# Optimization experiments

Hardware: AMD Instinct MI355X
Metric: run time of the kernel (lower is better)

## Reference

```python
import jax, jax.numpy as jnp
import numpy as np

B, S, D_IN, D_OUT = 4, 2048, 4096, 4096


def setup_inputs() -> dict:
    key = jax.random.key(0)
    k1, k2, k3, k4 = jax.random.split(key, 4)
    x = jax.random.normal(k1, (B, S, D_IN), dtype=jnp.float32) * 0.02
    base = jax.random.normal(k2, (D_IN, D_OUT), dtype=jnp.float32) * 0.02
    # mask holds the sign bits of the weight delta: 1 -> +1, 0 -> -1
    mask = jax.random.randint(k3, (D_IN, D_OUT), 0, 2, dtype=jnp.int32)
    # coeff = mean(|diff|); a small positive scalar
    coeff = jnp.abs(jax.random.normal(k4, (), dtype=jnp.float32)) * 0.01
    return {"x": x, "base": base, "coeff": coeff, "mask": mask}


def reference(x, base, coeff, mask):
    # binary_bmm(x, packed_mask) == x @ sign, sign = 2*mask - 1 in {-1, +1}
    sign = (2 * mask - 1).astype(x.dtype)            # [D_IN, D_OUT]
    return x @ base + coeff * (x @ sign)             # [B, S, D_OUT]
```

## Files before the change

kernel.cpp:

```cpp
#include <hip/hip_runtime.h>
#include <hip/hip_bf16.h>
#include <stdint.h>

#define M_DIM 8192
#define K_DIM 4096
#define N_DIM 4096
#define NT (K_DIM / 64)

typedef __attribute__((ext_vector_type(8))) short short8;
typedef __attribute__((ext_vector_type(4))) float f32x4;
typedef unsigned short ushort_t;

typedef const __attribute__((address_space(1))) unsigned int as1const_u32;
typedef __attribute__((address_space(3))) unsigned int as3_u32;

__device__ __forceinline__ unsigned short f2bf(float f) {
  unsigned int u = __float_as_uint(f);
  u += 0x7FFF + ((u >> 16) & 1);
  return (unsigned short)(u >> 16);
}

__global__ void cvt_x_kernel(const float* __restrict__ x,
                             ushort_t* __restrict__ xb, long n8) {
  long i = (long)blockIdx.x * blockDim.x + threadIdx.x;
  long stride = (long)gridDim.x * blockDim.x;
  for (; i < n8; i += stride) {
    const float4* p = (const float4*)(x + i * 8);
    float4 v0 = p[0], v1 = p[1];
    short8 o;
    o[0] = (short)f2bf(v0.x); o[1] = (short)f2bf(v0.y);
    o[2] = (short)f2bf(v0.z); o[3] = (short)f2bf(v0.w);
    o[4] = (short)f2bf(v1.x); o[5] = (short)f2bf(v1.y);
    o[6] = (short)f2bf(v1.z); o[7] = (short)f2bf(v1.w);
    *(short8*)(xb + i * 8) = o;
  }
}

__global__ void make_wt_kernel(const float* __restrict__ base,
                               const int* __restrict__ mask,
                               const float* __restrict__ coeffp,
                               ushort_t* __restrict__ wt) {
  __shared__ ushort_t tile[32][33];
  const float c = *coeffp;
  const int n0 = blockIdx.x * 32, k0 = blockIdx.y * 32;
  const int tx = threadIdx.x, ty = threadIdx.y;
#pragma unroll
  for (int r = 0; r < 4; ++r) {
    int k = k0 + ty + r * 8;
    int n = n0 + tx;
    size_t idx = (size_t)k * N_DIM + n;
    float s = mask[idx] ? c : -c;
    tile[ty + r * 8][tx] = f2bf(base[idx] + s);
  }
  __syncthreads();
#pragma unroll
  for (int r = 0; r < 4; ++r) {
    int n = n0 + ty + r * 8;
    int k = k0 + tx;
    wt[(size_t)n * K_DIM + k] = tile[tx][ty + r * 8];
  }
}

#define FENCE asm volatile("" ::: "memory")
#define BAR   do { FENCE; __builtin_amdgcn_s_barrier(); FENCE; } while (0)
#define VW6   asm volatile("s_waitcnt vmcnt(6)" ::: "memory")
#define VW4   asm volatile("s_waitcnt vmcnt(4)" ::: "memory")
#define VW0   asm volatile("s_waitcnt vmcnt(0)" ::: "memory")

__global__ __launch_bounds__(512, 2) void gemm_bf16_256(
    const ushort_t* __restrict__ Xb,
    const ushort_t* __restrict__ Wt,
    float* __restrict__ out) {
  __shared__ ushort_t Al[2][256][64];
  __shared__ ushort_t Bl[2][256][64];

  const int tid = threadIdx.x;
  const int lane = tid & 63;
  const int w = tid >> 6;
  const int wm = w >> 2, wn = w & 3;
  const int lrow = lane & 15, kg = lane >> 4;

  const int bid = blockIdx.x;
  const int swz = (bid & 7) * 64 + (bid >> 3);
  const int bm = (swz >> 4) * 256;
  const int bn = (swz & 15) * 256;

  const int rh0 = w * 8 + (lane >> 3);
  const int srcslot = (lane & 7) ^ ((lane >> 3) & 7);
  const ushort_t* Ag = Xb + (size_t)(bm + rh0) * K_DIM + srcslot * 8;
  const ushort_t* Bg = Wt + (size_t)(bn + rh0) * K_DIM + srcslot * 8;
  char* AlB = (char*)&Al[0][0][0];
  char* BlB = (char*)&Bl[0][0][0];
  const int ldsw = w * 1024;

#define STAGE(Og, Lb, u, h) do {                                                   \
    const ushort_t* _s0 = (Og) + (size_t)((h) * 128) * K_DIM + (size_t)(u) * 64;   \
    __builtin_amdgcn_global_load_lds((as1const_u32*)_s0,                           \
        (as3_u32*)((Lb) + ((u) & 1) * 32768 + (h) * 16384 + ldsw), 16, 0, 0);      \
    __builtin_amdgcn_global_load_lds((as1const_u32*)(_s0 + (size_t)64 * K_DIM),    \
        (as3_u32*)((Lb) + ((u) & 1) * 32768 + (h) * 16384 + ldsw + 8192), 16, 0, 0); \
  } while (0)

  const int arow = (wm * 16 + lrow) << 7;
  const int brow = (wn * 16 + lrow) << 7;
  const int sw0 = ((0 + kg) ^ (lrow & 7)) << 4;
  const int sw1 = ((4 + kg) ^ (lrow & 7)) << 4;

#define LDA(bt, mi, kk) (*(const short8*)(AlB + (bt) * 32768 + (mi) * 4096 + arow + ((kk) ? sw1 : sw0)))
#define LDB(bt, ni, kk) (*(const short8*)(BlB + (bt) * 32768 + (ni) * 8192 + brow + ((kk) ? sw1 : sw0)))
#define MFMA(a, b, c) __builtin_amdgcn_mfma_f32_16x16x32_bf16(a, b, c, 0, 0, 0)

  short8 Ar0[4][2], Ar1[4][2];
  short8 Br0[2][2], Br1[2][2];
  f32x4 acc[8][4] = {};

#define RD_A(dst, bt, base)                                                        \
  _Pragma("unroll")                                                                \
  for (int mi = 0; mi < 4; ++mi) {                                                 \
    dst[mi][0] = LDA(bt, (base) + mi, 0); dst[mi][1] = LDA(bt, (base) + mi, 1);    \
  }
#define RD_B(dst, bt, base)                                                        \
  _Pragma("unroll")                                                                \
  for (int ni = 0; ni < 2; ++ni) {                                                 \
    dst[ni][0] = LDB(bt, (base) + ni, 0); dst[ni][1] = LDB(bt, (base) + ni, 1);    \
  }
#define MMQ(mb, nb, Aset, Bset)                                                    \
  _Pragma("unroll")                                                                \
  for (int mi = 0; mi < 4; ++mi)                                                   \
    _Pragma("unroll")                                                              \
    for (int ni = 0; ni < 2; ++ni) {                                               \
      acc[(mb) + mi][(nb) + ni] = MFMA(Aset[mi][0], Bset[ni][0], acc[(mb) + mi][(nb) + ni]); \
      acc[(mb) + mi][(nb) + ni] = MFMA(Aset[mi][1], Bset[ni][1], acc[(mb) + mi][(nb) + ni]); \
    }

  STAGE(Ag, AlB, 0, 0); STAGE(Bg, BlB, 0, 0);
  STAGE(Bg, BlB, 0, 1); STAGE(Ag, AlB, 0, 1);
  STAGE(Ag, AlB, 1, 0); STAGE(Bg, BlB, 1, 0);
  VW4; BAR;
  RD_A(Ar0, 0, 0);
  RD_B(Br0, 0, 0);

  for (int t = 0; t < NT - 2; ++t) {
    const int bt = t & 1, bo = bt ^ 1;

    RD_B(Br1, bt, 2);
    STAGE(Bg, BlB, t + 1, 1);
    BAR;
    __builtin_amdgcn_s_setprio(1);
    MMQ(0, 0, Ar0, Br0);
    __builtin_amdgcn_s_setprio(0);
    VW6; BAR;

    RD_A(Ar1, bt, 4);
    STAGE(Ag, AlB, t + 1, 1);
    BAR;
    __builtin_amdgcn_s_setprio(1);
    MMQ(0, 2, Ar0, Br1);
    __builtin_amdgcn_s_setprio(0);
    VW6; BAR;

    STAGE(Ag, AlB, t + 2, 0);
    BAR;
    __builtin_amdgcn_s_setprio(1);
    MMQ(4, 0, Ar1, Br0);
    __builtin_amdgcn_s_setprio(0);
    RD_A(Ar0, bo, 0);
    BAR;

    STAGE(Bg, BlB, t + 2, 0);
    BAR;
    __builtin_amdgcn_s_setprio(1);
    MMQ(4, 2, Ar1, Br1);
    __builtin_amdgcn_s_setprio(0);
    VW6;
    RD_B(Br0, bo, 0);
    BAR;
  }

  STAGE(Bg, BlB, NT - 1, 1);
  STAGE(Ag, AlB, NT - 1, 1);
  VW0; BAR;
  {
    const int bt = (NT - 2) & 1, bl = (NT - 1) & 1;
    RD_B(Br1, bt, 2);
    RD_A(Ar1, bt, 4);
    MMQ(0, 0, Ar0, Br0);
    MMQ(0, 2, Ar0, Br1);
    MMQ(4, 0, Ar1, Br0);
    MMQ(4, 2, Ar1, Br1);
    RD_A(Ar0, bl, 0);
    RD_B(Br0, bl, 0);
    RD_B(Br1, bl, 2);
    RD_A(Ar1, bl, 4);
    MMQ(0, 0, Ar0, Br0);
    MMQ(0, 2, Ar0, Br1);
    MMQ(4, 0, Ar1, Br0);
    MMQ(4, 2, Ar1, Br1);
  }

#pragma unroll
  for (int mi = 0; mi < 8; ++mi)
#pragma unroll
    for (int ni = 0; ni < 4; ++ni) {
      const int gr = bm + mi * 32 + wm * 16 + kg * 4;
      const int gc = bn + ni * 64 + wn * 16 + lrow;
      float* o = out + (size_t)gr * N_DIM + gc;
#pragma unroll
      for (int r = 0; r < 4; ++r) o[(size_t)r * N_DIM] = acc[mi][ni][r];
    }
}

__global__ void gemm_f32_fallback(const float* __restrict__ x,
                                  const float* __restrict__ base,
                                  const float* __restrict__ coeffp,
                                  const int* __restrict__ mask,
                                  float* __restrict__ out) {
  __shared__ float As[32][33];
  __shared__ float Bs[32][33];
  const float c = *coeffp;
  const int tx = threadIdx.x, ty = threadIdx.y;
  const int row = blockIdx.y * 32 + ty, col = blockIdx.x * 32 + tx;
  float acc = 0.f;
  for (int kt = 0; kt < K_DIM; kt += 32) {
    As[ty][tx] = x[(size_t)row * K_DIM + kt + tx];
    size_t bidx = (size_t)(kt + ty) * N_DIM + col;
    Bs[ty][tx] = base[bidx] + (mask[bidx] ? c : -c);
    __syncthreads();
#pragma unroll
    for (int k = 0; k < 32; ++k) acc += As[ty][k] * Bs[k][tx];
    __syncthreads();
  }
  out[(size_t)row * N_DIM + col] = acc;
}

extern "C" void kernel_launch(void* const* d_in, const int* in_sizes, int n_in,
                              void* d_out, int out_size, void* d_ws, size_t ws_size,
                              hipStream_t stream) {
  const float* x     = (const float*)d_in[0];
  const float* base  = (const float*)d_in[1];
  const float* coeff = (const float*)d_in[2];
  const int*   mask  = (const int*)d_in[3];
  float* out = (float*)d_out;

  const size_t xb_bytes = (size_t)M_DIM * K_DIM * sizeof(ushort_t);
  const size_t wt_bytes = (size_t)K_DIM * N_DIM * sizeof(ushort_t);

  if (ws_size >= xb_bytes + wt_bytes) {
    ushort_t* xb = (ushort_t*)d_ws;
    ushort_t* wt = (ushort_t*)((char*)d_ws + xb_bytes);
    long n8 = (long)M_DIM * K_DIM / 8;
    cvt_x_kernel<<<4096, 256, 0, stream>>>(x, xb, n8);
    make_wt_kernel<<<dim3(N_DIM / 32, K_DIM / 32), dim3(32, 8), 0, stream>>>(base, mask, coeff, wt);
    gemm_bf16_256<<<512, 512, 0, stream>>>(xb, wt, out);
  } else {
    gemm_f32_fallback<<<dim3(N_DIM / 32, M_DIM / 32), dim3(32, 32), 0, stream>>>(x, base, coeff, mask, out);
  }
}
```

Baseline: 341.4 us.

## Restructure GEMM main loop to a simpler double-buffered schedule with fewer barriers

Replaces the four-phase interleaved schedule, where each quarter of the MFMA work sat between its own stage and barrier, with a per-iteration schedule. Each iteration reads all A/B fragments for the current buffer, runs half of the MFMAs, waits on lgkmcnt and one barrier, issues all global-to-LDS loads for tile t+2, then runs the remaining MFMAs. The prologue preloads two full tiles and the epilogue is split around a vmcnt(0) wait. This cuts the barriers per iteration from eight to two and reduces fine-grained waits. In exchange, LDS reads and global loads overlap with MFMA work at coarser granularity, which may expose more LDS latency.

```diff
diff --git a/kernel.cpp b/kernel.cpp
--- a/kernel.cpp
+++ b/kernel.cpp
@@ -63,9 +63,9 @@
 
 #define FENCE asm volatile("" ::: "memory")
 #define BAR   do { FENCE; __builtin_amdgcn_s_barrier(); FENCE; } while (0)
-#define VW6   asm volatile("s_waitcnt vmcnt(6)" ::: "memory")
-#define VW4   asm volatile("s_waitcnt vmcnt(4)" ::: "memory")
+#define VW8   asm volatile("s_waitcnt vmcnt(8)" ::: "memory")
 #define VW0   asm volatile("s_waitcnt vmcnt(0)" ::: "memory")
+#define LGK0  asm volatile("s_waitcnt lgkmcnt(0)" ::: "memory")
 
 __global__ __launch_bounds__(512, 2) void gemm_bf16_256(
     const ushort_t* __restrict__ Xb,
@@ -110,9 +110,9 @@
 #define LDB(bt, ni, kk) (*(const short8*)(BlB + (bt) * 32768 + (ni) * 8192 + brow + ((kk) ? sw1 : sw0)))
 #define MFMA(a, b, c) __builtin_amdgcn_mfma_f32_16x16x32_bf16(a, b, c, 0, 0, 0)
 
+  f32x4 acc[8][4] = {};
   short8 Ar0[4][2], Ar1[4][2];
   short8 Br0[2][2], Br1[2][2];
-  f32x4 acc[8][4] = {};
 
 #define RD_A(dst, bt, base)                                                        \
   _Pragma("unroll")                                                                \
@@ -134,64 +134,51 @@
     }
 
   STAGE(Ag, AlB, 0, 0); STAGE(Bg, BlB, 0, 0);
-  STAGE(Bg, BlB, 0, 1); STAGE(Ag, AlB, 0, 1);
+  STAGE(Ag, AlB, 0, 1); STAGE(Bg, BlB, 0, 1);
   STAGE(Ag, AlB, 1, 0); STAGE(Bg, BlB, 1, 0);
-  VW4; BAR;
-  RD_A(Ar0, 0, 0);
-  RD_B(Br0, 0, 0);
+  STAGE(Ag, AlB, 1, 1); STAGE(Bg, BlB, 1, 1);
+  VW8; BAR;
 
   for (int t = 0; t < NT - 2; ++t) {
-    const int bt = t & 1, bo = bt ^ 1;
-
-    RD_B(Br1, bt, 2);
-    STAGE(Bg, BlB, t + 1, 1);
-    BAR;
+    const int bt = t & 1;
+
+    RD_A(Ar0, bt, 0);
+    RD_B(Br0, bt, 0);
     __builtin_amdgcn_s_setprio(1);
     MMQ(0, 0, Ar0, Br0);
     __builtin_amdgcn_s_setprio(0);
-    VW6; BAR;
-
+    RD_B(Br1, bt, 2);
     RD_A(Ar1, bt, 4);
-    STAGE(Ag, AlB, t + 1, 1);
-    BAR;
     __builtin_amdgcn_s_setprio(1);
     MMQ(0, 2, Ar0, Br1);
     __builtin_amdgcn_s_setprio(0);
-    VW6; BAR;
-
-    STAGE(Ag, AlB, t + 2, 0);
-    BAR;
+
+    LGK0; BAR;
+    STAGE(Ag, AlB, t + 2, 0); STAGE(Bg, BlB, t + 2, 0);
+    STAGE(Ag, AlB, t + 2, 1); STAGE(Bg, BlB, t + 2, 1);
+
     __builtin_amdgcn_s_setprio(1);
     MMQ(4, 0, Ar1, Br0);
-    __builtin_amdgcn_s_setprio(0);
-    RD_A(Ar0, bo, 0);
-    BAR;
-
-    STAGE(Bg, BlB, t + 2, 0);
-    BAR;
-    __builtin_amdgcn_s_setprio(1);
     MMQ(4, 2, Ar1, Br1);
     __builtin_amdgcn_s_setprio(0);
-    VW6;
-    RD_B(Br0, bo, 0);
-    BAR;
-  }
-
-  STAGE(Bg, BlB, NT - 1, 1);
-  STAGE(Ag, AlB, NT - 1, 1);
-  VW0; BAR;
+
+    VW8; BAR;
+  }
+
   {
-    const int bt = (NT - 2) & 1, bl = (NT - 1) & 1;
-    RD_B(Br1, bt, 2);
-    RD_A(Ar1, bt, 4);
+    const int bt = (NT - 2) & 1;
+    RD_A(Ar0, bt, 0); RD_B(Br0, bt, 0);
+    RD_B(Br1, bt, 2); RD_A(Ar1, bt, 4);
     MMQ(0, 0, Ar0, Br0);
     MMQ(0, 2, Ar0, Br1);
     MMQ(4, 0, Ar1, Br0);
     MMQ(4, 2, Ar1, Br1);
-    RD_A(Ar0, bl, 0);
-    RD_B(Br0, bl, 0);
-    RD_B(Br1, bl, 2);
-    RD_A(Ar1, bl, 4);
+  }
+  VW0; BAR;
+  {
+    const int bt = (NT - 1) & 1;
+    RD_A(Ar0, bt, 0); RD_B(Br0, bt, 0);
+    RD_B(Br1, bt, 2); RD_A(Ar1, bt, 4);
     MMQ(0, 0, Ar0, Br0);
     MMQ(0, 2, Ar0, Br1);
     MMQ(4, 0, Ar1, Br0);
```

After: 330.9 us. 1.03x faster.

## Switch GEMM inner loop to 32x32x16 bf16 MFMA tiles

Applied to the files above, without the earlier changes.

Replaces the 16x16x32 MFMA micro-tiles with 32x32x16 MFMA instructions. The LDS fragment reads, register blocking, pipeline phases and output store mapping are restructured to match. This aims to cut LDS read traffic per flop and issue overhead by using larger MFMA tiles with fewer instructions. The accumulator layout changes to 16-float vectors, and the restructured barrier and wait schedule could reduce how well loads overlap with math.

```diff
diff --git a/kernel.cpp b/kernel.cpp
--- a/kernel.cpp
+++ b/kernel.cpp
@@ -8,7 +8,7 @@
 #define NT (K_DIM / 64)
 
 typedef __attribute__((ext_vector_type(8))) short short8;
-typedef __attribute__((ext_vector_type(4))) float f32x4;
+typedef __attribute__((ext_vector_type(16))) float f32x16;
 typedef unsigned short ushort_t;
 
 typedef const __attribute__((address_space(1))) unsigned int as1const_u32;
@@ -64,7 +64,6 @@
 #define FENCE asm volatile("" ::: "memory")
 #define BAR   do { FENCE; __builtin_amdgcn_s_barrier(); FENCE; } while (0)
 #define VW6   asm volatile("s_waitcnt vmcnt(6)" ::: "memory")
-#define VW4   asm volatile("s_waitcnt vmcnt(4)" ::: "memory")
 #define VW0   asm volatile("s_waitcnt vmcnt(0)" ::: "memory")
 
 __global__ __launch_bounds__(512, 2) void gemm_bf16_256(
@@ -78,7 +77,7 @@
   const int lane = tid & 63;
   const int w = tid >> 6;
   const int wm = w >> 2, wn = w & 3;
-  const int lrow = lane & 15, kg = lane >> 4;
+  const int l31 = lane & 31, l5 = lane >> 5;
 
   const int bid = blockIdx.x;
   const int swz = (bid & 7) * 64 + (bid >> 3);
@@ -101,112 +100,105 @@
         (as3_u32*)((Lb) + ((u) & 1) * 32768 + (h) * 16384 + ldsw + 8192), 16, 0, 0); \
   } while (0)
 
-  const int arow = (wm * 16 + lrow) << 7;
-  const int brow = (wn * 16 + lrow) << 7;
-  const int sw0 = ((0 + kg) ^ (lrow & 7)) << 4;
-  const int sw1 = ((4 + kg) ^ (lrow & 7)) << 4;
-
-#define LDA(bt, mi, kk) (*(const short8*)(AlB + (bt) * 32768 + (mi) * 4096 + arow + ((kk) ? sw1 : sw0)))
-#define LDB(bt, ni, kk) (*(const short8*)(BlB + (bt) * 32768 + (ni) * 8192 + brow + ((kk) ? sw1 : sw0)))
-#define MFMA(a, b, c) __builtin_amdgcn_mfma_f32_16x16x32_bf16(a, b, c, 0, 0, 0)
-
-  short8 Ar0[4][2], Ar1[4][2];
-  short8 Br0[2][2], Br1[2][2];
-  f32x4 acc[8][4] = {};
-
-#define RD_A(dst, bt, base)                                                        \
+  const int arow = (wm * 32 + l31) << 7;
+  const int brow = (wn * 32 + l31) << 7;
+  const int sw32[4] = { (((0 * 2 + l5) ^ (lane & 7)) << 4),
+                        (((1 * 2 + l5) ^ (lane & 7)) << 4),
+                        (((2 * 2 + l5) ^ (lane & 7)) << 4),
+                        (((3 * 2 + l5) ^ (lane & 7)) << 4) };
+
+#define LDA32(bt, mi, kk) (*(const short8*)(AlB + (bt) * 32768 + (mi) * 8192 + arow + sw32[kk]))
+#define LDB32(bt, ni, kk) (*(const short8*)(BlB + (bt) * 32768 + (ni) * 16384 + brow + sw32[kk]))
+#define MFMA32(a, b, c) __builtin_amdgcn_mfma_f32_32x32x16_bf16(a, b, c, 0, 0, 0)
+
+  f32x16 acc[4][2] = {};
+  short8 Ar[2][4];
+  short8 Br0[4], Br1[4];
+
+#define RD_A2(bt, mi0)                                                             \
   _Pragma("unroll")                                                                \
-  for (int mi = 0; mi < 4; ++mi) {                                                 \
-    dst[mi][0] = LDA(bt, (base) + mi, 0); dst[mi][1] = LDA(bt, (base) + mi, 1);    \
-  }
-#define RD_B(dst, bt, base)                                                        \
+  for (int mi = 0; mi < 2; ++mi)                                                   \
+    _Pragma("unroll")                                                              \
+    for (int kk = 0; kk < 4; ++kk) Ar[mi][kk] = LDA32(bt, (mi0) + mi, kk);
+#define RD_B(dst, bt, ni)                                                          \
   _Pragma("unroll")                                                                \
-  for (int ni = 0; ni < 2; ++ni) {                                                 \
-    dst[ni][0] = LDB(bt, (base) + ni, 0); dst[ni][1] = LDB(bt, (base) + ni, 1);    \
-  }
-#define MMQ(mb, nb, Aset, Bset)                                                    \
+  for (int kk = 0; kk < 4; ++kk) dst[kk] = LDB32(bt, ni, kk);
+#define MMQ32(mb, nb, Bset)                                                        \
   _Pragma("unroll")                                                                \
-  for (int mi = 0; mi < 4; ++mi)                                                   \
+  for (int kk = 0; kk < 4; ++kk)                                                   \
     _Pragma("unroll")                                                              \
-    for (int ni = 0; ni < 2; ++ni) {                                               \
-      acc[(mb) + mi][(nb) + ni] = MFMA(Aset[mi][0], Bset[ni][0], acc[(mb) + mi][(nb) + ni]); \
-      acc[(mb) + mi][(nb) + ni] = MFMA(Aset[mi][1], Bset[ni][1], acc[(mb) + mi][(nb) + ni]); \
-    }
+    for (int mi = 0; mi < 2; ++mi)                                                 \
+      acc[(mb) + mi][nb] = MFMA32(Ar[mi][kk], Bset[kk], acc[(mb) + mi][nb]);
 
   STAGE(Ag, AlB, 0, 0); STAGE(Bg, BlB, 0, 0);
   STAGE(Bg, BlB, 0, 1); STAGE(Ag, AlB, 0, 1);
   STAGE(Ag, AlB, 1, 0); STAGE(Bg, BlB, 1, 0);
-  VW4; BAR;
-  RD_A(Ar0, 0, 0);
-  RD_B(Br0, 0, 0);
+  VW6; BAR;
 
   for (int t = 0; t < NT - 2; ++t) {
-    const int bt = t & 1, bo = bt ^ 1;
-
-    RD_B(Br1, bt, 2);
+    const int bt = t & 1;
+
+    RD_A2(bt, 0);
+    RD_B(Br0, bt, 0);
     STAGE(Bg, BlB, t + 1, 1);
     BAR;
     __builtin_amdgcn_s_setprio(1);
-    MMQ(0, 0, Ar0, Br0);
+    MMQ32(0, 0, Br0);
+    __builtin_amdgcn_s_setprio(0);
+    BAR;
+
+    RD_B(Br1, bt, 1);
+    STAGE(Ag, AlB, t + 1, 1);
+    BAR;
+    __builtin_amdgcn_s_setprio(1);
+    MMQ32(0, 1, Br1);
     __builtin_amdgcn_s_setprio(0);
     VW6; BAR;
 
-    RD_A(Ar1, bt, 4);
-    STAGE(Ag, AlB, t + 1, 1);
-    BAR;
-    __builtin_amdgcn_s_setprio(1);
-    MMQ(0, 2, Ar0, Br1);
+    RD_A2(bt, 2);
+    STAGE(Ag, AlB, t + 2, 0);
+    BAR;
+    __builtin_amdgcn_s_setprio(1);
+    MMQ32(2, 0, Br0);
+    __builtin_amdgcn_s_setprio(0);
+    BAR;
+
+    STAGE(Bg, BlB, t + 2, 0);
+    BAR;
+    __builtin_amdgcn_s_setprio(1);
+    MMQ32(2, 1, Br1);
     __builtin_amdgcn_s_setprio(0);
     VW6; BAR;
-
-    STAGE(Ag, AlB, t + 2, 0);
-    BAR;
-    __builtin_amdgcn_s_setprio(1);
-    MMQ(4, 0, Ar1, Br0);
-    __builtin_amdgcn_s_setprio(0);
-    RD_A(Ar0, bo, 0);
-    BAR;
-
-    STAGE(Bg, BlB, t + 2, 0);
-    BAR;
-    __builtin_amdgcn_s_setprio(1);
-    MMQ(4, 2, Ar1, Br1);
-    __builtin_amdgcn_s_setprio(0);
-    VW6;
-    RD_B(Br0, bo, 0);
-    BAR;
   }
 
   STAGE(Bg, BlB, NT - 1, 1);
   STAGE(Ag, AlB, NT - 1, 1);
   VW0; BAR;
-  {
-    const int bt = (NT - 2) & 1, bl = (NT - 1) & 1;
-    RD_B(Br1, bt, 2);
-    RD_A(Ar1, bt, 4);
-    MMQ(0, 0, Ar0, Br0);
-    MMQ(0, 2, Ar0, Br1);
-    MMQ(4, 0, Ar1, Br0);
-    MMQ(4, 2, Ar1, Br1);
-    RD_A(Ar0, bl, 0);
-    RD_B(Br0, bl, 0);
-    RD_B(Br1, bl, 2);
-    RD_A(Ar1, bl, 4);
-    MMQ(0, 0, Ar0, Br0);
-    MMQ(0, 2, Ar0, Br1);
-    MMQ(4, 0, Ar1, Br0);
-    MMQ(4, 2, Ar1, Br1);
-  }
-
-#pragma unroll
-  for (int mi = 0; mi < 8; ++mi)
-#pragma unroll
-    for (int ni = 0; ni < 4; ++ni) {
-      const int gr = bm + mi * 32 + wm * 16 + kg * 4;
-      const int gc = bn + ni * 64 + wn * 16 + lrow;
+#pragma unroll
+  for (int tt = 0; tt < 2; ++tt) {
+    const int bt = (NT - 2 + tt) & 1;
+    RD_A2(bt, 0);
+    RD_B(Br0, bt, 0);
+    RD_B(Br1, bt, 1);
+    MMQ32(0, 0, Br0);
+    MMQ32(0, 1, Br1);
+    RD_A2(bt, 2);
+    MMQ32(2, 0, Br0);
+    MMQ32(2, 1, Br1);
+  }
+
+#pragma unroll
+  for (int mi = 0; mi < 4; ++mi)
+#pragma unroll
+    for (int ni = 0; ni < 2; ++ni) {
+      const int gr = bm + mi * 64 + wm * 32 + l5 * 4;
+      const int gc = bn + ni * 128 + wn * 32 + l31;
       float* o = out + (size_t)gr * N_DIM + gc;
 #pragma unroll
-      for (int r = 0; r < 4; ++r) o[(size_t)r * N_DIM] = acc[mi][ni][r];
+      for (int r = 0; r < 16; ++r) {
+        const int rowf = (r & 3) + 8 * (r >> 2);
+        o[(size_t)rowf * N_DIM] = acc[mi][ni][r];
+      }
     }
 }
 
```

Result: no change. 335.8 us (-1.6%).
